# Kernel optimization log

Hardware: AMD Instinct MI355X
Metric: run time of the kernel (lower is better)

## Reference

```python
import jax, jax.numpy as jnp
from jax import lax
import numpy as np

B, L, C, PRED = 64, 512, 321, 96
PATCH, STRIDE = 16, 8
N = (L - PATCH) // STRIDE + 1 + 1  # 64 patches (after replication pad)
HID = PATCH * 2                    # expansion_factor=2
ALPHA, EPS = 0.2, 1e-5

def gelu(v):
    return jax.nn.gelu(v, approximate=False)  # torch nn.GELU default (erf)

def setup_inputs() -> dict:
    key = jax.random.key(0)
    ks = jax.random.split(key, 10)
    init = lambda k, s: (jax.random.normal(k, s) * 0.02).astype(jnp.float32)
    return dict(
        x=jax.random.normal(ks[0], (B, L, C), jnp.float32),
        rev_w=jnp.ones((C,), jnp.float32), rev_b=jnp.zeros((C,), jnp.float32),
        fc1_w=init(ks[1], (HID, PATCH)), fc1_b=jnp.zeros((HID,), jnp.float32),
        bn1_w=jnp.ones((N,), jnp.float32), bn1_b=jnp.zeros((N,), jnp.float32),
        conv_w=init(ks[2], (N, 1, 3)), conv_b=jnp.zeros((N,), jnp.float32),
        bn2_w=jnp.ones((N,), jnp.float32), bn2_b=jnp.zeros((N,), jnp.float32),
        fc2_w=init(ks[3], (PATCH, HID)), fc2_b=jnp.zeros((PATCH,), jnp.float32),
        m1_w=init(ks[4], (2 * N, N)), m1_b=jnp.zeros((2 * N,), jnp.float32),
        m2_w=init(ks[5], (N, 2 * N)), m2_b=jnp.zeros((N,), jnp.float32),
        gl_scale=jnp.full((1,), 0.1, jnp.float32),
        ln_w=jnp.ones((PATCH,), jnp.float32), ln_b=jnp.zeros((PATCH,), jnp.float32),
        seas_w=init(ks[6], (PRED, N * PATCH)), seas_b=jnp.zeros((PRED,), jnp.float32),
        tr_w=init(ks[7], (PRED, L)), tr_b=jnp.zeros((PRED,), jnp.float32),
        fus_w=init(ks[8], (PRED, 2 * PRED)), fus_b=jnp.zeros((PRED,), jnp.float32),
    )

def _batchnorm(h, w, b):
    # BatchNorm1d over channel axis N (train-mode batch stats, biased var)
    mu = h.mean((0, 2), keepdims=True)
    var = h.var((0, 2), keepdims=True)
    return (h - mu) * lax.rsqrt(var + EPS) * w[None, :, None] + b[None, :, None]

def reference(x, rev_w, rev_b, fc1_w, fc1_b, bn1_w, bn1_b, conv_w, conv_b,
              bn2_w, bn2_b, fc2_w, fc2_b, m1_w, m1_b, m2_w, m2_b, gl_scale,
              ln_w, ln_b, seas_w, seas_b, tr_w, tr_b, fus_w, fus_b):
    # --- RevIN norm (torch std is unbiased, ddof=1) ---
    mean = x.mean(1, keepdims=True)
    std = jnp.std(x, axis=1, ddof=1, keepdims=True) + EPS
    xn = (x - mean) / std * rev_w + rev_b
    # --- EMA trend/seasonal decomposition via scan ---
    xt = jnp.moveaxis(xn, 1, 0)                      # [L,B,C]
    def step(c, xi):
        t = ALPHA * xi + (1.0 - ALPHA) * c
        return t, t
    _, rest = lax.scan(step, xt[0], xt[1:])
    trend = jnp.moveaxis(jnp.concatenate([xt[:1], rest], 0), 0, 1)  # [B,L,C]
    seasonal = xn - trend
    # --- patching (replication pad right by STRIDE, unfold) ---
    s = seasonal.transpose(0, 2, 1).reshape(B * C, L)
    s = jnp.concatenate([s, jnp.broadcast_to(s[:, -1:], (B * C, STRIDE))], axis=1)
    idx = np.arange(N)[:, None] * STRIDE + np.arange(PATCH)[None, :]
    sp = s[:, idx]                                    # [B*C, N, PATCH]
    # --- IntraPatch (local): fc1 -> GELU -> BN -> depthwise conv -> GELU -> BN -> fc2 + res ---
    h = gelu(sp @ fc1_w.T + fc1_b)                    # [BC,N,HID]
    h = _batchnorm(h, bn1_w, bn1_b)
    h = lax.conv_general_dilated(h, conv_w, (1,), ((1, 1),),
                                 feature_group_count=N,
                                 dimension_numbers=('NCH', 'OIH', 'NCH'))
    h = h + conv_b[None, :, None]
    h = _batchnorm(gelu(h), bn2_w, bn2_b)
    local = h @ fc2_w.T + fc2_b + sp                  # dropout is identity (eval)
    # --- InterPatch (global): pool -> MLP -> sigmoid gate ---
    pooled = sp.mean(-1)                              # [BC,N]
    w = jax.nn.sigmoid(gelu(pooled @ m1_w.T + m1_b) @ m2_w.T + m2_b)
    glob = sp * (1.0 + gl_scale * w[..., None])
    # --- fusion 'add' + residual LayerNorm over PATCH ---
    y = sp + local + glob
    mu = y.mean(-1, keepdims=True)
    var = y.var(-1, keepdims=True)
    y = (y - mu) * lax.rsqrt(var + EPS) * ln_w + ln_b
    # --- heads ---
    s_pred = y.reshape(B * C, N * PATCH) @ seas_w.T + seas_b
    t = trend.transpose(0, 2, 1).reshape(B * C, L)
    t_pred = t @ tr_w.T + tr_b
    out = jnp.concatenate([s_pred, t_pred], -1) @ fus_w.T + fus_b
    out = out.reshape(B, C, PRED).transpose(0, 2, 1)  # [B,PRED,C]
    # --- RevIN denorm ---
    out = (out - rev_b) / rev_w
    return out * std + mean
```

## Files before the change

### kernel.cpp

```cpp
#include <hip/hip_runtime.h>
#include <hip/hip_bf16.h>
#include <math.h>

#define B_    64
#define L_    512
#define C_    321
#define PRED_ 96
#define N_    64
#define HID_  32
#define BC_   (B_*C_)
#define SROW_ 528
#define EPS_  1e-5f
#define ALPHA_ 0.2f
#define GR_   16
#define RB_   8
#define NBLK2_ (BC_/GR_)
#define NBLKH_ (BC_/8)
#define D64_  6.2771017353866808e-7f
#define STW_  548
#define UTW_  260

typedef __attribute__((ext_vector_type(8))) short bf16x8;
typedef __attribute__((ext_vector_type(4))) float f32x4;

__device__ __forceinline__ float gelu_f(float x){
  float ax = fabsf(x);
  float z  = ax * 0.70710678118654752440f;
  float t  = __builtin_amdgcn_rcpf(fmaf(0.3275911f, z, 1.0f));
  float poly = fmaf(fmaf(fmaf(fmaf(1.061405429f, t, -1.453152027f),
                   t, 1.421413741f), t, -0.284496736f), t, 0.254829592f) * t;
  float e  = __expf(-z*z);
  float erfp = fmaf(-poly, e, 1.0f);
  return fmaf(0.5f*ax, erfp, 0.5f*x);
}
__device__ __forceinline__ unsigned short bf16bits(float x){
  __hip_bfloat16 h = __float2bfloat16(x);
  return *(unsigned short*)&h;
}

__global__ __launch_bounds__(256) void k1_all(
    const float* __restrict__ x, const float* __restrict__ rev_w, const float* __restrict__ rev_b,
    const float* __restrict__ seas_w, const float* __restrict__ tr_w, const float* __restrict__ fus_w,
    const float* __restrict__ seas_b, const float* __restrict__ tr_b, const float* __restrict__ fus_b,
    float* __restrict__ s_raw, __hip_bfloat16* __restrict__ t_bf, float* __restrict__ rowpar,
    float* __restrict__ pooled,
    __hip_bfloat16* __restrict__ Wsf, __hip_bfloat16* __restrict__ Wtf,
    float* __restrict__ biasc, float* __restrict__ colsumT) {
  __shared__ float lf[8][32];
  __shared__ float psum[8][32], psq[8][32];
  __shared__ float fs[8][32];
  __shared__ float st[32*STW_];
  int tid = threadIdx.x;
  int bid = blockIdx.x;
  if (bid >= BC_/32) {
    int fb = bid - BC_/32;
    if (fb < 576) {
      int idx = fb*256 + tid;
      int j = idx / 1536, k = idx - j*1536;
      float acc = 0.f;
      if (k < 1024) {
        for (int i=0;i<96;++i) acc = fmaf(fus_w[j*192+i], seas_w[i*1024+k], acc);
        Wsf[(size_t)j*1024 + k] = __float2bfloat16(acc);
      } else {
        int l = k - 1024;
        for (int i=0;i<96;++i) acc = fmaf(fus_w[j*192+96+i], tr_w[i*512+l], acc);
        Wtf[(size_t)j*512 + l] = __float2bfloat16(acc);
      }
    } else {
      __shared__ float rowsum[96];
      if (tid < 96) {
        float s = 0.f;
        for (int l=0;l<512;++l) s += tr_w[tid*512+l];
        rowsum[tid] = s;
      }
      __syncthreads();
      if (tid < 96) {
        float acc = fus_b[tid], cs = 0.f;
        for (int i=0;i<96;++i) {
          acc = fmaf(fus_w[tid*192+i],    seas_b[i], acc);
          acc = fmaf(fus_w[tid*192+96+i], tr_b[i],   acc);
          cs  = fmaf(fus_w[tid*192+96+i], rowsum[i], cs);
        }
        biasc[tid] = acc; colsumT[tid] = cs;
      }
    }
    return;
  }
  int q = tid >> 5, r = tid & 31;
  int row0 = bid*32;
  int row = row0 + r;
  int b = row / C_, c = row - b*C_;
  const float* xp = x + (size_t)b*L_*C_ + c;
  int l0 = q*64;
  float sreg[64];
  float loc = 0.f, sum = 0.f, sq = 0.f;
  #pragma unroll
  for (int i=0;i<64;++i) {
    float v = xp[(size_t)(l0+i)*C_];
    sum += v; sq = fmaf(v,v,sq);
    loc = (q==0 && i==0) ? v : fmaf(ALPHA_, v, 0.8f*loc);
    sreg[i] = loc;
  }
  lf[q][r] = loc; psum[q][r] = sum; psq[q][r] = sq;
  __syncthreads();
  float cin = 0.f;
  for (int j=0;j<q;++j) cin = fmaf(D64_, cin, lf[j][r]);
  float S=0.f, Q=0.f;
  #pragma unroll
  for (int qq=0;qq<8;++qq){ S += psum[qq][r]; Q += psq[qq][r]; }
  float mean = S*(1.0f/512.0f);
  float var  = (Q - S*S*(1.0f/512.0f))*(1.0f/511.0f);
  var = fmaxf(var, 0.f);
  float stdv = sqrtf(var) + EPS_;
  float rwc = rev_w[c];
  float a = rwc / stdv;
  if (q==0) {
    float rbc = rev_b[c];
    float g = rbc - mean*a;
    float inva = stdv / rwc;
    ((float4*)rowpar)[row] = make_float4(a, g, mean, inva);
  }
  float prev = 0.f, f = 1.f, slast = 0.f;
  float sums8[8];
  #pragma unroll
  for (int j=0;j<8;++j) sums8[j] = 0.f;
  #pragma unroll
  for (int i=0;i<64;++i) {
    float lc = sreg[i];
    f *= 0.8f;
    float s = (q==0 && i==0) ? 0.f : fmaf(4.f, lc - prev, -f*cin);
    prev = lc;
    float sv = s * a;
    st[r*STW_ + q*64 + i] = sv;
    sums8[i>>3] += sv;
    slast = sv;
  }
  fs[q][r] = sums8[0];
  if (q==7) {
    #pragma unroll
    for (int k=0;k<8;++k) st[r*STW_ + 512 + k] = slast;
  }
  __syncthreads();
  for (int idx=tid; idx<32*130; idx+=256) {
    int rr = idx/130, g = idx - rr*130;
    float4 v = *(float4*)&st[rr*STW_ + g*4];
    *(float4*)&s_raw[(size_t)(row0+rr)*SROW_ + g*4] = v;
  }
  {
    float nf = (q < 7) ? fs[q+1][r] : 8.0f*slast;
    #pragma unroll
    for (int j=0;j<7;++j)
      pooled[(size_t)row*64 + q*8 + j] = (sums8[j] + sums8[j+1])*(1.0f/16.0f);
    pooled[(size_t)row*64 + q*8 + 7] = (sums8[7] + nf)*(1.0f/16.0f);
  }
  __syncthreads();
  unsigned* tb = (unsigned*)st;
  {
    float f2 = 1.f; unsigned lo = 0;
    #pragma unroll
    for (int i=0;i<64;++i) {
      f2 *= 0.8f;
      float tt = fmaf(f2, cin, sreg[i]) * a;
      unsigned hb = bf16bits(tt);
      if ((i&1)==0) lo = hb;
      else tb[r*UTW_ + q*32 + (i>>1)] = lo | (hb<<16);
    }
  }
  __syncthreads();
  for (int idx=tid; idx<32*64; idx+=256) {
    int rr = idx>>6, g = idx&63;
    uint4 v = *(uint4*)&tb[rr*UTW_ + g*4];
    *(uint4*)&t_bf[(size_t)(row0+rr)*512 + g*8] = v;
  }
}

__global__ __launch_bounds__(512) void k4_gate(
    const float* __restrict__ pooled,
    const float* __restrict__ m1_w, const float* __restrict__ m1_b,
    const float* __restrict__ m2_w, const float* __restrict__ m2_b,
    float* __restrict__ wl_g) {
  __shared__ __align__(16) __hip_bfloat16 buf[17408];
  int t = threadIdx.x;
  int row0 = blockIdx.x*64;
  __hip_bfloat16* A1 = buf;
  __hip_bfloat16* B1 = buf + 4608;
  __hip_bfloat16* H1 = buf;
  __hip_bfloat16* B2 = buf + 8704;
  for (int idx=t; idx<4096; idx+=512) {
    int r = idx>>6, k = idx&63;
    A1[r*72+k] = __float2bfloat16(pooled[(size_t)(row0+r)*64 + k]);
  }
  for (int idx=t; idx<8192; idx+=512) {
    int r = idx>>6, k = idx&63;
    B1[r*72+k] = __float2bfloat16(m1_w[idx]);
  }
  __syncthreads();
  int lane = t & 63, w = t >> 6;
  int fr = lane & 15, fg = lane >> 4;
  int mt = w & 3;
  int ng0 = (w>>2)*4;
  f32x4 acc1[4];
  #pragma unroll
  for (int nn=0;nn<4;++nn) acc1[nn] = (f32x4){0.f,0.f,0.f,0.f};
  #pragma unroll
  for (int ksub=0; ksub<2; ++ksub) {
    bf16x8 av = *(bf16x8*)&A1[(mt*16+fr)*72 + ksub*32 + fg*8];
    #pragma unroll
    for (int nn=0;nn<4;++nn) {
      bf16x8 bv = *(bf16x8*)&B1[((ng0+nn)*16+fr)*72 + ksub*32 + fg*8];
      acc1[nn] = __builtin_amdgcn_mfma_f32_16x16x32_bf16(av, bv, acc1[nn], 0,0,0);
    }
  }
  __syncthreads();
  #pragma unroll
  for (int nn=0;nn<4;++nn) {
    int col = (ng0+nn)*16 + fr;
    float bias = m1_b[col];
    #pragma unroll
    for (int reg=0;reg<4;++reg) {
      int row = mt*16 + fg*4 + reg;
      H1[row*136 + col] = __float2bfloat16(gelu_f(acc1[nn][reg] + bias));
    }
  }
  for (int idx=t; idx<8192; idx+=512) {
    int r = idx>>7, k = idx&127;
    B2[r*136+k] = __float2bfloat16(m2_w[idx]);
  }
  __syncthreads();
  int nt0 = (w>>2)*2;
  f32x4 acc2[2];
  #pragma unroll
  for (int nn=0;nn<2;++nn) acc2[nn] = (f32x4){0.f,0.f,0.f,0.f};
  #pragma unroll
  for (int ksub=0; ksub<4; ++ksub) {
    bf16x8 av = *(bf16x8*)&H1[(mt*16+fr)*136 + ksub*32 + fg*8];
    #pragma unroll
    for (int nn=0;nn<2;++nn) {
      bf16x8 bv = *(bf16x8*)&B2[((nt0+nn)*16+fr)*136 + ksub*32 + fg*8];
      acc2[nn] = __builtin_amdgcn_mfma_f32_16x16x32_bf16(av, bv, acc2[nn], 0,0,0);
    }
  }
  #pragma unroll
  for (int nn=0;nn<2;++nn) {
    int col = (nt0+nn)*16 + fr;
    float bias = m2_b[col];
    #pragma unroll
    for (int reg=0;reg<4;++reg) {
      int row = mt*16 + fg*4 + reg;
      wl_g[(size_t)(row0+row)*64 + col] = 1.0f/(1.0f + __expf(-(acc2[nn][reg] + bias)));
    }
  }
}

__global__ __launch_bounds__(256) void k2_bn1stats(
    const float* __restrict__ s_raw,
    const float* __restrict__ fc1_w, const float* __restrict__ fc1_b,
    float* __restrict__ partials) {
  __shared__ float sl[GR_*SROW_];
  __shared__ float red[2][GR_*64];
  int t = threadIdx.x;
  int row0 = blockIdx.x*GR_;
  for (int idx=t; idx<GR_*520; idx+=256) {
    int rr = idx/520, cc = idx - rr*520;
    sl[rr*SROW_+cc] = s_raw[(size_t)(row0+rr)*SROW_+cc];
  }
  __syncthreads();
  int lr = t >> 4, ng = t & 15;
  for (int q=0;q<4;++q) {
    int n = ng + 16*q;
    float sp[16];
    #pragma unroll
    for (int p=0;p<16;++p) sp[p] = sl[lr*SROW_ + n*8 + p];
    float s1=0.f, s2=0.f;
    #pragma unroll
    for (int hid=0; hid<32; ++hid) {
      float acc = fc1_b[hid];
      #pragma unroll
      for (int p=0;p<16;++p) acc = fmaf(sp[p], fc1_w[hid*16+p], acc);
      float gv = gelu_f(acc);
      s1 += gv; s2 = fmaf(gv,gv,s2);
    }
    red[0][lr*64+n] = s1;
    red[1][lr*64+n] = s2;
  }
  __syncthreads();
  if (t < 64) {
    float S1=0.f, S2=0.f;
    for (int lr2=0; lr2<GR_; ++lr2) { S1 += red[0][lr2*64+t]; S2 += red[1][lr2*64+t]; }
    partials[((size_t)blockIdx.x*64+t)*2+0] = S1;
    partials[((size_t)blockIdx.x*64+t)*2+1] = S2;
  }
}

__global__ __launch_bounds__(512) void k2v2_bn1_cr(
    const float* __restrict__ s_raw,
    const float* __restrict__ fc1_w, const float* __restrict__ fc1_b,
    const float* __restrict__ conv_w,
    float* __restrict__ partials, __hip_bfloat16* __restrict__ crp) {
  __shared__ float cw[192];
  __shared__ float red[2][512];
  int t = threadIdx.x;
  int row0 = blockIdx.x*8;
  if (t < 192) cw[t] = conv_w[t];
  __syncthreads();
  int lr = t>>6, n = t&63;
  const float* sp_g = &s_raw[(size_t)(row0+lr)*SROW_ + n*8];
  float sp[16];
  {
    float4 v0 = *(const float4*)(sp_g);
    float4 v1 = *(const float4*)(sp_g+4);
    float4 v2 = *(const float4*)(sp_g+8);
    float4 v3 = *(const float4*)(sp_g+12);
    sp[0]=v0.x; sp[1]=v0.y; sp[2]=v0.z; sp[3]=v0.w;
    sp[4]=v1.x; sp[5]=v1.y; sp[6]=v1.z; sp[7]=v1.w;
    sp[8]=v2.x; sp[9]=v2.y; sp[10]=v2.z; sp[11]=v2.w;
    sp[12]=v3.x; sp[13]=v3.y; sp[14]=v3.z; sp[15]=v3.w;
  }
  float w0=cw[n*3], wm=cw[n*3+1], wp=cw[n*3+2];
  float s1=0.f, s2=0.f;
  auto gf = [&](int k)->float {
    float acc = fc1_b[k];
    #pragma unroll
    for (int p=0;p<16;++p) acc = fmaf(sp[p], fc1_w[k*16+p], acc);
    float g = gelu_f(acc);
    s1 += g; s2 = fmaf(g,g,s2);
    return g;
  };
  float gm = 0.f, gc = gf(0), gp = gf(1);
  unsigned wds[16]; unsigned crlo = 0;
  #pragma unroll
  for (int k=0;k<32;++k) {
    float cr = fmaf(gm, w0, fmaf(gc, wm, (k<31) ? gp*wp : 0.f));
    unsigned hb = bf16bits(cr);
    if ((k&1)==0) crlo = hb; else wds[k>>1] = crlo | (hb<<16);
    gm = gc; gc = gp;
    gp = (k+2<32) ? gf(k+2) : 0.f;
  }
  uint4* dst = (uint4*)&crp[((size_t)(row0+lr)*64 + n)*32];
  dst[0] = make_uint4(wds[0],wds[1],wds[2],wds[3]);
  dst[1] = make_uint4(wds[4],wds[5],wds[6],wds[7]);
  dst[2] = make_uint4(wds[8],wds[9],wds[10],wds[11]);
  dst[3] = make_uint4(wds[12],wds[13],wds[14],wds[15]);
  red[0][t] = s1;
  red[1][t] = s2;
  __syncthreads();
  if (t < 64) {
    float S1=0.f, S2=0.f;
    #pragma unroll
    for (int lr2=0; lr2<8; ++lr2) { S1 += red[0][lr2*64+t]; S2 += red[1][lr2*64+t]; }
    partials[((size_t)blockIdx.x*64+t)*2+0] = S1;
    partials[((size_t)blockIdx.x*64+t)*2+1] = S2;
  }
}

__global__ __launch_bounds__(256) void k_bnreduce(
    const float* __restrict__ partials, int nblk,
    const float* __restrict__ bnw, const float* __restrict__ bnb,
    float* __restrict__ scale, float* __restrict__ shift) {
  __shared__ float red[2][256];
  int n = blockIdx.x, t = threadIdx.x;
  float s1=0.f, s2=0.f;
  for (int i=t; i<nblk; i+=256) {
    s1 += partials[((size_t)i*64+n)*2+0];
    s2 += partials[((size_t)i*64+n)*2+1];
  }
  red[0][t]=s1; red[1][t]=s2;
  __syncthreads();
  for (int off=128; off>0; off>>=1) {
    if (t<off) { red[0][t]+=red[0][t+off]; red[1][t]+=red[1][t+off]; }
    __syncthreads();
  }
  if (t==0) {
    const float count = (float)BC_ * 32.0f;
    float mu = red[0][0]/count;
    float var = red[1][0]/count - mu*mu;
    float sc = rsqrtf(var + EPS_) * bnw[n];
    scale[n] = sc;
    shift[n] = bnb[n] - mu*sc;
  }
}

__global__ __launch_bounds__(256) void k3_bn2stats(
    const float* __restrict__ s_raw,
    const float* __restrict__ fc1_w, const float* __restrict__ fc1_b,
    const float* __restrict__ scale1, const float* __restrict__ shift1,
    const float* __restrict__ conv_w, const float* __restrict__ conv_b,
    float* __restrict__ partials) {
  __shared__ float sl[GR_*SROW_];
  __shared__ float sc1[64], sh1[64], cw[192], cb[64];
  __shared__ float red[2][GR_*64];
  int t = threadIdx.x;
  int row0 = blockIdx.x*GR_;
  if (t < 64) { sc1[t]=scale1[t]; sh1[t]=shift1[t]; cb[t]=conv_b[t]; }
  if (t >= 64 && t < 256) cw[t-64] = conv_w[t-64];
  __syncthreads();
  for (int idx=t; idx<GR_*520; idx+=256) {
    int rr = idx/520, cc = idx - rr*520;
    sl[rr*SROW_+cc] = s_raw[(size_t)(row0+rr)*SROW_+cc];
  }
  __syncthreads();
  int lr = t >> 4, ng = t & 15;
  for (int q=0;q<4;++q) {
    int n = ng + 16*q;
    float sp[16];
    #pragma unroll
    for (int p=0;p<16;++p) sp[p] = sl[lr*SROW_ + n*8 + p];
    float scn = sc1[n], shn = sh1[n];
    float h[32];
    #pragma unroll
    for (int hid=0; hid<32; ++hid) {
      float acc = fc1_b[hid];
      #pragma unroll
      for (int p=0;p<16;++p) acc = fmaf(sp[p], fc1_w[hid*16+p], acc);
      h[hid] = fmaf(gelu_f(acc), scn, shn);
    }
    float w0=cw[n*3], wm=cw[n*3+1], wpp=cw[n*3+2], cbn=cb[n];
    float s1=0.f, s2=0.f, prev=0.f;
    #pragma unroll
    for (int k2=0;k2<32;++k2) {
      float cur = h[k2];
      float cv = cbn;
      cv = fmaf(prev, w0, cv);
      cv = fmaf(cur, wm, cv);
      if (k2<31) cv = fmaf(h[k2+1], wpp, cv);
      float gv = gelu_f(cv);
      s1 += gv; s2 = fmaf(gv,gv,s2);
      prev = cur;
    }
    red[0][lr*64+n]=s1; red[1][lr*64+n]=s2;
  }
  __syncthreads();
  if (t < 64) {
    float S1=0.f, S2=0.f;
    for (int lr2=0; lr2<GR_; ++lr2) { S1 += red[0][lr2*64+t]; S2 += red[1][lr2*64+t]; }
    partials[((size_t)blockIdx.x*64+t)*2+0] = S1;
    partials[((size_t)blockIdx.x*64+t)*2+1] = S2;
  }
}

__global__ __launch_bounds__(512) void k3v2_bn2stats(
    const __hip_bfloat16* __restrict__ crp,
    const float* __restrict__ scale1, const float* __restrict__ shift1,
    const float* __restrict__ conv_w, const float* __restrict__ conv_b,
    float* __restrict__ partials) {
  __shared__ float sc1[64], sh0l[64], shml[64], sh31l[64];
  __shared__ float red[2][512];
  int t = threadIdx.x;
  int row0 = blockIdx.x*8;
  if (t < 64) {
    float w0=conv_w[t*3], wm=conv_w[t*3+1], wp=conv_w[t*3+2];
    float s1v=shift1[t], cbv=conv_b[t];
    sc1[t]  = scale1[t];
    sh0l[t] = fmaf(s1v, wm+wp, cbv);
    shml[t] = fmaf(s1v, w0+wm+wp, cbv);
    sh31l[t]= fmaf(s1v, w0+wm, cbv);
  }
  __syncthreads();
  int lr = t>>6, n = t&63;
  const uint4* crb = (const uint4*)&crp[((size_t)(row0+lr)*64 + n)*32];
  uint4 u0=crb[0], u1=crb[1], u2=crb[2], u3=crb[3];
  unsigned uw[16] = {u0.x,u0.y,u0.z,u0.w, u1.x,u1.y,u1.z,u1.w,
                     u2.x,u2.y,u2.z,u2.w, u3.x,u3.y,u3.z,u3.w};
  float sc1n = sc1[n];
  float shm = shml[n];
  float s1=0.f, s2=0.f;
  #pragma unroll
  for (int j=0;j<16;++j) {
    unsigned u = uw[j];
    float c0 = __uint_as_float(u<<16);
    float c1 = __uint_as_float(u & 0xffff0000u);
    float sh_0 = (j==0)  ? sh0l[n]  : shm;
    float sh_1 = (j==15) ? sh31l[n] : shm;
    float g0 = gelu_f(fmaf(c0, sc1n, sh_0));
    float g1 = gelu_f(fmaf(c1, sc1n, sh_1));
    s1 += g0 + g1;
    s2 = fmaf(g0,g0, fmaf(g1,g1, s2));
  }
  red[0][t]=s1; red[1][t]=s2;
  __syncthreads();
  if (t < 64) {
    float S1=0.f, S2=0.f;
    #pragma unroll
    for (int lr2=0; lr2<8; ++lr2) { S1 += red[0][lr2*64+t]; S2 += red[1][lr2*64+t]; }
    partials[((size_t)blockIdx.x*64+t)*2+0] = S1;
    partials[((size_t)blockIdx.x*64+t)*2+1] = S2;
  }
}

__global__ __launch_bounds__(256) void k5a_pipeline(
    const float* __restrict__ s_raw, const float* __restrict__ wl_g,
    const float* __restrict__ fc1_w, const float* __restrict__ fc1_b,
    const float* __restrict__ scale1, const float* __restrict__ shift1,
    const float* __restrict__ conv_w, const float* __restrict__ conv_b,
    const float* __restrict__ scale2, const float* __restrict__ shift2,
    const float* __restrict__ fc2_w, const float* __restrict__ fc2_b,
    const float* __restrict__ gl_scale,
    const float* __restrict__ ln_w, const float* __restrict__ ln_b,
    __hip_bfloat16* __restrict__ ybf) {
  __shared__ float sl[RB_*SROW_];
  __shared__ float cw[192], cb[64];
  __shared__ float sc1[64], sh1[64], sc2[64], sh2[64];
  int t = threadIdx.x;
  int row0 = blockIdx.x*RB_;
  if (t<64) { sc1[t]=scale1[t]; sh1[t]=shift1[t]; sc2[t]=scale2[t]; sh2[t]=shift2[t]; cb[t]=conv_b[t]; }
  if (t>=64 && t<256) cw[t-64]=conv_w[t-64];
  __syncthreads();
  for (int idx=t; idx<RB_*520; idx+=256) {
    int rr = idx/520, cc = idx - rr*520;
    sl[rr*SROW_+cc] = s_raw[(size_t)(row0+rr)*SROW_+cc];
  }
  __syncthreads();
  float glv = gl_scale[0];
  for (int idx=t; idx<RB_*64; idx+=256) {
    int rr = idx>>6, n = idx&63;
    float wlv = wl_g[(size_t)row0*64 + idx];
    float h[32];
    {
      float sp[16];
      #pragma unroll
      for (int p=0;p<16;++p) sp[p] = sl[rr*SROW_ + n*8 + p];
      float scn=sc1[n], shn=sh1[n];
      #pragma unroll
      for (int hid=0;hid<32;++hid) {
        float acc=fc1_b[hid];
        #pragma unroll
        for (int p=0;p<16;++p) acc=fmaf(sp[p], fc1_w[hid*16+p], acc);
        h[hid]=fmaf(gelu_f(acc), scn, shn);
      }
    }
    {
      float w0=cw[n*3], wm=cw[n*3+1], wpp=cw[n*3+2], cbn=cb[n];
      float sc2n=sc2[n], sh2n=sh2[n];
      float prev=0.f;
      #pragma unroll
      for (int k2=0;k2<32;++k2) {
        float cur = h[k2];
        float cv = cbn;
        cv = fmaf(prev, w0, cv);
        cv = fmaf(cur, wm, cv);
        if (k2<31) cv = fmaf(h[k2+1], wpp, cv);
        h[k2] = fmaf(gelu_f(cv), sc2n, sh2n);
        prev = cur;
      }
    }
    float yv[16];
    #pragma unroll
    for (int p=0;p<16;++p) {
      float acc=fc2_b[p];
      #pragma unroll
      for (int hid=0;hid<32;++hid) acc=fmaf(h[hid], fc2_w[p*32+hid], acc);
      yv[p]=acc;
    }
    float smul = 3.0f + glv*wlv;
    float mu=0.f;
    #pragma unroll
    for (int p=0;p<16;++p) {
      yv[p]=fmaf(sl[rr*SROW_ + n*8 + p], smul, yv[p]);
      mu+=yv[p];
    }
    mu *= (1.0f/16.0f);
    float var=0.f;
    #pragma unroll
    for (int p=0;p<16;++p){ float d=yv[p]-mu; var=fmaf(d,d,var); }
    var *= (1.0f/16.0f);
    float rs = rsqrtf(var + EPS_);
    unsigned int wds[8];
    #pragma unroll
    for (int j=0;j<8;++j) {
      unsigned int lo = bf16bits(fmaf((yv[2*j]-mu)*rs,   ln_w[2*j],   ln_b[2*j]));
      unsigned int hi = bf16bits(fmaf((yv[2*j+1]-mu)*rs, ln_w[2*j+1], ln_b[2*j+1]));
      wds[j] = lo | (hi<<16);
    }
    size_t ybase = (size_t)(row0+rr)*1024 + n*16;
    uint4* dst = (uint4*)&ybf[ybase];
    dst[0] = make_uint4(wds[0],wds[1],wds[2],wds[3]);
    dst[1] = make_uint4(wds[4],wds[5],wds[6],wds[7]);
  }
}

__global__ __launch_bounds__(512) void k5a_v2(
    const float* __restrict__ s_raw, const float* __restrict__ wl_g,
    const __hip_bfloat16* __restrict__ crp,
    const float* __restrict__ scale1, const float* __restrict__ shift1,
    const float* __restrict__ conv_w, const float* __restrict__ conv_b,
    const float* __restrict__ scale2, const float* __restrict__ shift2,
    const float* __restrict__ fc2_w, const float* __restrict__ fc2_b,
    const float* __restrict__ gl_scale,
    const float* __restrict__ ln_w, const float* __restrict__ ln_b,
    __hip_bfloat16* __restrict__ ybf) {
  __shared__ float sl[RB_*SROW_];
  __shared__ float sc1[64], sh0l[64], shml[64], sh31l[64], sc2[64], sh2[64];
  int t = threadIdx.x;
  int row0 = blockIdx.x*RB_;
  if (t < 64) {
    float w0=conv_w[t*3], wm=conv_w[t*3+1], wp=conv_w[t*3+2];
    float s1v=shift1[t], cbv=conv_b[t];
    sc1[t]  = scale1[t];
    sh0l[t] = fmaf(s1v, wm+wp, cbv);
    shml[t] = fmaf(s1v, w0+wm+wp, cbv);
    sh31l[t]= fmaf(s1v, w0+wm, cbv);
    sc2[t]=scale2[t]; sh2[t]=shift2[t];
  }
  __syncthreads();
  for (int idx=t; idx<RB_*520; idx+=512) {
    int rr = idx/520, cc = idx - rr*520;
    sl[rr*SROW_+cc] = s_raw[(size_t)(row0+rr)*SROW_+cc];
  }
  __syncthreads();
  float glv = gl_scale[0];
  {
    int idx = t;
    int rr = idx>>6, n = idx&63;
    float wlv = wl_g[(size_t)row0*64 + idx];
    const uint4* crb = (const uint4*)&crp[((size_t)(row0+rr)*64 + n)*32];
    uint4 u0=crb[0], u1=crb[1], u2=crb[2], u3=crb[3];
    unsigned uw[16] = {u0.x,u0.y,u0.z,u0.w, u1.x,u1.y,u1.z,u1.w,
                       u2.x,u2.y,u2.z,u2.w, u3.x,u3.y,u3.z,u3.w};
    float sc1n = sc1[n], sc2n = sc2[n], sh2n = sh2[n];
    float shm = shml[n];
    float yv[16];
    #pragma unroll
    for (int p=0;p<16;++p) yv[p] = fc2_b[p];
    #pragma unroll
    for (int j=0;j<16;++j) {
      unsigned u = uw[j];
      int k0 = 2*j, k1 = 2*j+1;
      float c0 = __uint_as_float(u<<16);
      float c1 = __uint_as_float(u & 0xffff0000u);
      float sh_0 = (j==0)  ? sh0l[n]  : shm;
      float sh_1 = (j==15) ? sh31l[n] : shm;
      float h2a = fmaf(gelu_f(fmaf(c0, sc1n, sh_0)), sc2n, sh2n);
      float h2b = fmaf(gelu_f(fmaf(c1, sc1n, sh_1)), sc2n, sh2n);
      #pragma unroll
      for (int p=0;p<16;++p)
        yv[p] = fmaf(h2a, fc2_w[p*32+k0], fmaf(h2b, fc2_w[p*32+k1], yv[p]));
    }
    float smul = 3.0f + glv*wlv;
    float mu=0.f;
    #pragma unroll
    for (int p=0;p<16;++p) {
      yv[p] = fmaf(sl[rr*SROW_ + n*8 + p], smul, yv[p]);
      mu += yv[p];
    }
    mu *= (1.0f/16.0f);
    float var=0.f;
    #pragma unroll
    for (int p=0;p<16;++p){ float d=yv[p]-mu; var=fmaf(d,d,var); }
    var *= (1.0f/16.0f);
    float rs = rsqrtf(var + EPS_);
    unsigned int wds[8];
    #pragma unroll
    for (int j=0;j<8;++j) {
      unsigned int lo = bf16bits(fmaf((yv[2*j]-mu)*rs,   ln_w[2*j],   ln_b[2*j]));
      unsigned int hi = bf16bits(fmaf((yv[2*j+1]-mu)*rs, ln_w[2*j+1], ln_b[2*j+1]));
      wds[j] = lo | (hi<<16);
    }
    size_t ybase = (size_t)(row0+rr)*1024 + n*16;
    uint4* dst = (uint4*)&ybf[ybase];
    dst[0] = make_uint4(wds[0],wds[1],wds[2],wds[3]);
    dst[1] = make_uint4(wds[4],wds[5],wds[6],wds[7]);
  }
}

__global__ __launch_bounds__(256) void k5b_gemm(
    const __hip_bfloat16* __restrict__ ybf, const __hip_bfloat16* __restrict__ tbf,
    const __hip_bfloat16* __restrict__ Wsf, const __hip_bfloat16* __restrict__ Wtf,
    const float* __restrict__ rowpar, const float* __restrict__ rev_b,
    const float* __restrict__ biasc, const float* __restrict__ colsumT,
    float* __restrict__ out) {
  __shared__ __align__(16) __hip_bfloat16 As[2*32*72];
  __shared__ __align__(16) __hip_bfloat16 Bs[2*96*72];
  __shared__ float rp[128];
  __shared__ float rbl[32];
  __shared__ int   obase[32];
  __shared__ float bcl[96], csl[96];
  int tid = threadIdx.x;
  int row0 = blockIdx.x*32;
  if (tid < 128) rp[tid] = rowpar[(size_t)row0*4 + tid];
  if (tid >= 128 && tid < 160) {
    int lr = tid-128;
    int row = row0 + lr; int b = row/C_; int c = row - b*C_;
    rbl[lr] = rev_b[c]; obase[lr] = b*PRED_*C_ + c;
  }
  if (tid >= 160 && tid < 256) { bcl[tid-160]=biasc[tid-160]; csl[tid-160]=colsumT[tid-160]; }
  int lane = tid & 63, w = tid >> 6;
  int fr = lane & 15, fg = lane >> 4;
  int wr = w & 1, wc = w >> 1;
  int ra = tid>>3, ca = tid&7;
  int rb0 = tid>>3,       cb0_ = tid&7;
  int rb1 = (tid+256)>>3, cb1_ = (tid+256)&7;
  int rb2 = (tid+512)>>3, cb2_ = (tid+512)&7;
  f32x4 acc[3];
  #pragma unroll
  for (int n=0;n<3;++n) acc[n] = (f32x4){0.f,0.f,0.f,0.f};

  uint4 ar, br[3];
  auto LOAD = [&](int ks){
    if (ks < 8) {
      int kofs = ks*64;
      ar    = *(const uint4*)&tbf[(size_t)(row0+ra)*512 + kofs + ca*8];
      br[0] = *(const uint4*)&Wtf[(size_t)rb0*512 + kofs + cb0_*8];
      br[1] = *(const uint4*)&Wtf[(size_t)rb1*512 + kofs + cb1_*8];
      br[2] = *(const uint4*)&Wtf[(size_t)rb2*512 + kofs + cb2_*8];
    } else {
      int kofs = (ks-8)*64;
      ar    = *(const uint4*)&ybf[(size_t)(row0+ra)*1024 + kofs + ca*8];
      br[0] = *(const uint4*)&Wsf[(size_t)rb0*1024 + kofs + cb0_*8];
      br[1] = *(const uint4*)&Wsf[(size_t)rb1*1024 + kofs + cb1_*8];
      br[2] = *(const uint4*)&Wsf[(size_t)rb2*1024 + kofs + cb2_*8];
    }
  };

  LOAD(0);
  int cur = 0;
  for (int ks=0; ks<24; ++ks) {
    __hip_bfloat16* Ab = &As[cur*32*72];
    __hip_bfloat16* Bb = &Bs[cur*96*72];
    *(uint4*)&Ab[ra*72 + ca*8] = ar;
    *(uint4*)&Bb[rb0*72 + cb0_*8] = br[0];
    *(uint4*)&Bb[rb1*72 + cb1_*8] = br[1];
    *(uint4*)&Bb[rb2*72 + cb2_*8] = br[2];
    __syncthreads();
    if (ks < 23) LOAD(ks+1);
    #pragma unroll
    for (int ksub=0; ksub<2; ++ksub) {
      bf16x8 av = *(bf16x8*)&Ab[(wr*16+fr)*72 + ksub*32 + fg*8];
      #pragma unroll
      for (int nn=0;nn<3;++nn) {
        int n16 = wc*3 + nn;
        bf16x8 bv = *(bf16x8*)&Bb[(n16*16+fr)*72 + ksub*32 + fg*8];
        acc[nn] = __builtin_amdgcn_mfma_f32_16x16x32_bf16(av, bv, acc[nn], 0,0,0);
      }
    }
    cur ^= 1;
  }
  #pragma unroll
  for (int nn=0;nn<3;++nn) {
    int col = (wc*3+nn)*16 + fr;
    float cs = csl[col], bc = bcl[col];
    #pragma unroll
    for (int reg=0;reg<4;++reg) {
      int rloc = wr*16 + fg*4 + reg;
      float g = rp[rloc*4+1], meanv = rp[rloc*4+2], inva = rp[rloc*4+3];
      float val = acc[nn][reg] + g*cs + bc;
      val = (val - rbl[rloc])*inva + meanv;
      out[(size_t)obase[rloc] + (size_t)col*C_] = val;
    }
  }
}

extern "C" void kernel_launch(void* const* d_in, const int* in_sizes, int n_in,
                              void* d_out, int out_size, void* d_ws, size_t ws_size,
                              hipStream_t stream) {
  const float* x      = (const float*)d_in[0];
  const float* rev_w  = (const float*)d_in[1];
  const float* rev_b  = (const float*)d_in[2];
  const float* fc1_w  = (const float*)d_in[3];
  const float* fc1_b  = (const float*)d_in[4];
  const float* bn1_w  = (const float*)d_in[5];
  const float* bn1_b  = (const float*)d_in[6];
  const float* conv_w = (const float*)d_in[7];
  const float* conv_b = (const float*)d_in[8];
  const float* bn2_w  = (const float*)d_in[9];
  const float* bn2_b  = (const float*)d_in[10];
  const float* fc2_w  = (const float*)d_in[11];
  const float* fc2_b  = (const float*)d_in[12];
  const float* m1_w   = (const float*)d_in[13];
  const float* m1_b   = (const float*)d_in[14];
  const float* m2_w   = (const float*)d_in[15];
  const float* m2_b   = (const float*)d_in[16];
  const float* gl     = (const float*)d_in[17];
  const float* ln_w   = (const float*)d_in[18];
  const float* ln_b   = (const float*)d_in[19];
  const float* seas_w = (const float*)d_in[20];
  const float* seas_b = (const float*)d_in[21];
  const float* tr_w   = (const float*)d_in[22];
  const float* tr_b   = (const float*)d_in[23];
  const float* fus_w  = (const float*)d_in[24];
  const float* fus_b  = (const float*)d_in[25];
  float* out = (float*)d_out;
  float* ws = (float*)d_ws;

  __hip_bfloat16* Wsf  = (__hip_bfloat16*)(ws);
  __hip_bfloat16* Wtf  = (__hip_bfloat16*)(ws + 49152);
  float* biasc   = ws + 73728;
  float* colsumT = ws + 73856;
  float* scale1  = ws + 73984;
  float* shift1  = ws + 74048;
  float* scale2  = ws + 74112;
  float* shift2  = ws + 74176;
  float* partials= ws + 74240;
  float* rowpar  = ws + 238592;
  float* s_raw   = ws + 320768;
  __hip_bfloat16* t_bf = (__hip_bfloat16*)(ws + 11168000);
  __hip_bfloat16* ybf  = (__hip_bfloat16*)(ws + 16427264);
  float* pooled  = ws + 26945792;
  float* wl_g    = ws + 28260608;
  __hip_bfloat16* crp  = (__hip_bfloat16*)(ws + 29575424);
  float* pbig    = ws + 16427264;
  const size_t NEED = (29575424ull + 21037056ull) * 4ull;
  bool big = (ws_size >= NEED);

  hipLaunchKernelGGL(k1_all, dim3(BC_/32 + 577), dim3(256), 0, stream,
    x, rev_w, rev_b, seas_w, tr_w, fus_w, seas_b, tr_b, fus_b,
    s_raw, t_bf, rowpar, pooled, Wsf, Wtf, biasc, colsumT);
  hipLaunchKernelGGL(k4_gate, dim3(BC_/64), dim3(512), 0, stream, pooled, m1_w, m1_b, m2_w, m2_b, wl_g);
  if (big) {
    hipLaunchKernelGGL(k2v2_bn1_cr, dim3(NBLKH_), dim3(512), 0, stream, s_raw, fc1_w, fc1_b, conv_w, pbig, crp);
    hipLaunchKernelGGL(k_bnreduce, dim3(64), dim3(256), 0, stream, pbig, NBLKH_, bn1_w, bn1_b, scale1, shift1);
    hipLaunchKernelGGL(k3v2_bn2stats, dim3(NBLKH_), dim3(512), 0, stream, crp, scale1, shift1, conv_w, conv_b, pbig);
    hipLaunchKernelGGL(k_bnreduce, dim3(64), dim3(256), 0, stream, pbig, NBLKH_, bn2_w, bn2_b, scale2, shift2);
    hipLaunchKernelGGL(k5a_v2, dim3(BC_/RB_), dim3(512), 0, stream,
      s_raw, wl_g, crp, scale1, shift1, conv_w, conv_b,
      scale2, shift2, fc2_w, fc2_b, gl, ln_w, ln_b, ybf);
  } else {
    hipLaunchKernelGGL(k2_bn1stats, dim3(NBLK2_), dim3(256), 0, stream, s_raw, fc1_w, fc1_b, partials);
    hipLaunchKernelGGL(k_bnreduce, dim3(64), dim3(256), 0, stream, partials, NBLK2_, bn1_w, bn1_b, scale1, shift1);
    hipLaunchKernelGGL(k3_bn2stats, dim3(NBLK2_), dim3(256), 0, stream, s_raw, fc1_w, fc1_b, scale1, shift1, conv_w, conv_b, partials);
    hipLaunchKernelGGL(k_bnreduce, dim3(64), dim3(256), 0, stream, partials, NBLK2_, bn2_w, bn2_b, scale2, shift2);
    hipLaunchKernelGGL(k5a_pipeline, dim3(BC_/RB_), dim3(256), 0, stream,
      s_raw, wl_g, fc1_w, fc1_b, scale1, shift1, conv_w, conv_b,
      scale2, shift2, fc2_w, fc2_b, gl, ln_w, ln_b, ybf);
  }
  hipLaunchKernelGGL(k5b_gemm, dim3(BC_/32), dim3(256), 0, stream,
    ybf, t_bf, Wsf, Wtf, rowpar, rev_b, biasc, colsumT, out);
}
```

Before: 245.0 us.

## Load MFMA operands directly from global memory in head GEMM, dropping LDS staging

```diff
diff --git a/kernel.cpp b/kernel.cpp
--- a/kernel.cpp
+++ b/kernel.cpp
@@ -668,8 +668,6 @@
     const float* __restrict__ rowpar, const float* __restrict__ rev_b,
     const float* __restrict__ biasc, const float* __restrict__ colsumT,
     float* __restrict__ out) {
-  __shared__ __align__(16) __hip_bfloat16 As[2*32*72];
-  __shared__ __align__(16) __hip_bfloat16 Bs[2*96*72];
   __shared__ float rp[128];
   __shared__ float rbl[32];
   __shared__ int   obase[32];
@@ -683,56 +681,42 @@
     rbl[lr] = rev_b[c]; obase[lr] = b*PRED_*C_ + c;
   }
   if (tid >= 160 && tid < 256) { bcl[tid-160]=biasc[tid-160]; csl[tid-160]=colsumT[tid-160]; }
+  __syncthreads();
   int lane = tid & 63, w = tid >> 6;
   int fr = lane & 15, fg = lane >> 4;
   int wr = w & 1, wc = w >> 1;
-  int ra = tid>>3, ca = tid&7;
-  int rb0 = tid>>3,       cb0_ = tid&7;
-  int rb1 = (tid+256)>>3, cb1_ = (tid+256)&7;
-  int rb2 = (tid+512)>>3, cb2_ = (tid+512)&7;
   f32x4 acc[3];
   #pragma unroll
   for (int n=0;n<3;++n) acc[n] = (f32x4){0.f,0.f,0.f,0.f};
 
-  uint4 ar, br[3];
-  auto LOAD = [&](int ks){
-    if (ks < 8) {
-      int kofs = ks*64;
-      ar    = *(const uint4*)&tbf[(size_t)(row0+ra)*512 + kofs + ca*8];
-      br[0] = *(const uint4*)&Wtf[(size_t)rb0*512 + kofs + cb0_*8];
-      br[1] = *(const uint4*)&Wtf[(size_t)rb1*512 + kofs + cb1_*8];
-      br[2] = *(const uint4*)&Wtf[(size_t)rb2*512 + kofs + cb2_*8];
-    } else {
-      int kofs = (ks-8)*64;
-      ar    = *(const uint4*)&ybf[(size_t)(row0+ra)*1024 + kofs + ca*8];
-      br[0] = *(const uint4*)&Wsf[(size_t)rb0*1024 + kofs + cb0_*8];
-      br[1] = *(const uint4*)&Wsf[(size_t)rb1*1024 + kofs + cb1_*8];
-      br[2] = *(const uint4*)&Wsf[(size_t)rb2*1024 + kofs + cb2_*8];
-    }
-  };
-
-  LOAD(0);
-  int cur = 0;
-  for (int ks=0; ks<24; ++ks) {
-    __hip_bfloat16* Ab = &As[cur*32*72];
-    __hip_bfloat16* Bb = &Bs[cur*96*72];
-    *(uint4*)&Ab[ra*72 + ca*8] = ar;
-    *(uint4*)&Bb[rb0*72 + cb0_*8] = br[0];
-    *(uint4*)&Bb[rb1*72 + cb1_*8] = br[1];
-    *(uint4*)&Bb[rb2*72 + cb2_*8] = br[2];
-    __syncthreads();
-    if (ks < 23) LOAD(ks+1);
-    #pragma unroll
-    for (int ksub=0; ksub<2; ++ksub) {
-      bf16x8 av = *(bf16x8*)&Ab[(wr*16+fr)*72 + ksub*32 + fg*8];
-      #pragma unroll
-      for (int nn=0;nn<3;++nn) {
-        int n16 = wc*3 + nn;
-        bf16x8 bv = *(bf16x8*)&Bb[(n16*16+fr)*72 + ksub*32 + fg*8];
-        acc[nn] = __builtin_amdgcn_mfma_f32_16x16x32_bf16(av, bv, acc[nn], 0,0,0);
-      }
-    }
-    cur ^= 1;
+  const __hip_bfloat16* At = tbf + (size_t)(row0 + wr*16 + fr)*512 + fg*8;
+  const __hip_bfloat16* Ay = ybf + (size_t)(row0 + wr*16 + fr)*1024 + fg*8;
+  const __hip_bfloat16* Bt0 = Wtf + (size_t)((wc*3+0)*16 + fr)*512 + fg*8;
+  const __hip_bfloat16* Bt1 = Wtf + (size_t)((wc*3+1)*16 + fr)*512 + fg*8;
+  const __hip_bfloat16* Bt2 = Wtf + (size_t)((wc*3+2)*16 + fr)*512 + fg*8;
+  const __hip_bfloat16* By0 = Wsf + (size_t)((wc*3+0)*16 + fr)*1024 + fg*8;
+  const __hip_bfloat16* By1 = Wsf + (size_t)((wc*3+1)*16 + fr)*1024 + fg*8;
+  const __hip_bfloat16* By2 = Wsf + (size_t)((wc*3+2)*16 + fr)*1024 + fg*8;
+
+  #pragma unroll 4
+  for (int ks=0; ks<16; ++ks) {
+    bf16x8 av = *(const bf16x8*)(At + ks*32);
+    bf16x8 b0 = *(const bf16x8*)(Bt0 + ks*32);
+    bf16x8 b1 = *(const bf16x8*)(Bt1 + ks*32);
+    bf16x8 b2 = *(const bf16x8*)(Bt2 + ks*32);
+    acc[0] = __builtin_amdgcn_mfma_f32_16x16x32_bf16(av, b0, acc[0], 0,0,0);
+    acc[1] = __builtin_amdgcn_mfma_f32_16x16x32_bf16(av, b1, acc[1], 0,0,0);
+    acc[2] = __builtin_amdgcn_mfma_f32_16x16x32_bf16(av, b2, acc[2], 0,0,0);
+  }
+  #pragma unroll 4
+  for (int ks=0; ks<32; ++ks) {
+    bf16x8 av = *(const bf16x8*)(Ay + ks*32);
+    bf16x8 b0 = *(const bf16x8*)(By0 + ks*32);
+    bf16x8 b1 = *(const bf16x8*)(By1 + ks*32);
+    bf16x8 b2 = *(const bf16x8*)(By2 + ks*32);
+    acc[0] = __builtin_amdgcn_mfma_f32_16x16x32_bf16(av, b0, acc[0], 0,0,0);
+    acc[1] = __builtin_amdgcn_mfma_f32_16x16x32_bf16(av, b1, acc[1], 0,0,0);
+    acc[2] = __builtin_amdgcn_mfma_f32_16x16x32_bf16(av, b2, acc[2], 0,0,0);
   }
   #pragma unroll
   for (int nn=0;nn<3;++nn) {
```

After: 254.0 us. +3.7%, slower.
